# Kernel tuning notes

Hardware: AMD Instinct MI355X
Metric: run time of the kernel (lower is better)

The kernel has to match this reference:

```python
import jax, jax.numpy as jnp
import numpy as np

WINDOW = 8
HEADS = 8

def _rel_index(w):
    coords = np.stack(np.meshgrid(np.arange(w), np.arange(w), indexing='ij')).reshape(2, -1)
    rel = coords[:, :, None] - coords[:, None, :]          # [2, N, N]
    rel = rel.transpose(1, 2, 0) + (w - 1)                 # [N, N, 2]
    return jnp.asarray(rel[:, :, 0] * (2 * w - 1) + rel[:, :, 1])  # [N, N] int

def setup_inputs() -> dict:
    key = jax.random.key(0)
    ks = jax.random.split(key, 5)
    B, N, C = 4096, WINDOW * WINDOW, 256
    x = jax.random.normal(ks[0], (B, N, C), dtype=jnp.float32)
    w_qkv = jax.random.normal(ks[1], (3 * C, C), dtype=jnp.float32) * 0.02
    b_qkv = jnp.zeros((3 * C,), dtype=jnp.float32)
    bias_table = jax.random.normal(ks[2], ((2 * WINDOW - 1) ** 2, HEADS), dtype=jnp.float32) * 0.02
    w_proj = jax.random.normal(ks[3], (C, C), dtype=jnp.float32) * 0.02
    b_proj = jnp.zeros((C,), dtype=jnp.float32)
    return {"x": x, "w_qkv": w_qkv, "b_qkv": b_qkv, "bias_table": bias_table,
            "w_proj": w_proj, "b_proj": b_proj}

def reference(x, w_qkv, b_qkv, bias_table, w_proj, b_proj):
    B, N, C = x.shape
    H = HEADS
    d = C // H
    scale = d ** (-0.5)
    idx = _rel_index(WINDOW)                                # [N, N]
    qkv = x @ w_qkv.T + b_qkv                               # [B, N, 3C]
    qkv = qkv.reshape(B, N, 3, H, d).transpose(2, 0, 3, 1, 4)
    q, k, v = qkv[0], qkv[1], qkv[2]                        # [B, H, N, d]
    attn = jnp.einsum('bhnd,bhmd->bhnm', q * scale, k)      # [B, H, N, N]
    bias = bias_table[idx]                                  # [N, N, H]
    attn = attn + bias.transpose(2, 0, 1)[None]             # add per-head bias
    attn = jax.nn.softmax(attn, axis=-1)
    out = jnp.einsum('bhnm,bhmd->bhnd', attn, v)            # [B, H, N, d]
    out = out.transpose(0, 2, 1, 3).reshape(B, N, C)
    return out @ w_proj.T + b_proj
```

## Files before the change

### kernel.cpp

```cpp
#include <hip/hip_runtime.h>

typedef unsigned int u32;
typedef unsigned short u16;
typedef __bf16 bf16x8 __attribute__((ext_vector_type(8)));
typedef float f32x4 __attribute__((ext_vector_type(4)));
typedef u32 u32x4 __attribute__((ext_vector_type(4)));
typedef u32 u32x2 __attribute__((ext_vector_type(2)));

#define NTOK 64
#define CDIM 256
#define NH 8

#define WS_HDR 8
#define BIAS_O (WS_HDR)
#define WQKV_O (BIAS_O + 32768)
#define BQKV_O (WQKV_O + 196608)
#define WPRJ_O (BQKV_O + 768)
#define BPRJ_O (WPRJ_O + 65536)

#define XROW 520
#define LDS_BYTES 33280

__device__ __forceinline__ float bf2f(u16 u) {
  union { u32 i; float f; } z; z.i = ((u32)u) << 16; return z.f;
}
__device__ __forceinline__ u16 f2bf(float f) {
  __bf16 h = (__bf16)f; return __builtin_bit_cast(u16, h);
}
__device__ __forceinline__ u32 pk2(float a, float b) {
  return (u32)f2bf(a) | ((u32)f2bf(b) << 16);
}
__device__ __forceinline__ float fetchf(const void* p, int idx, int isbf) {
  return isbf ? bf2f(((const u16*)p)[idx]) : ((const float*)p)[idx];
}

__device__ __forceinline__ bf16x8 frag_from(u32 p00, u32 p01, u32 p10, u32 p11,
                                            int s0, int s1, bool hi) {
  u32 A0 = (u32)__shfl((int)p00, s0, 64);
  u32 A1 = (u32)__shfl((int)p01, s0, 64);
  u32 B0 = (u32)__shfl((int)p10, s0, 64);
  u32 B1 = (u32)__shfl((int)p11, s0, 64);
  u32 C0 = (u32)__shfl((int)p00, s1, 64);
  u32 C1 = (u32)__shfl((int)p01, s1, 64);
  u32 D0 = (u32)__shfl((int)p10, s1, 64);
  u32 D1 = (u32)__shfl((int)p11, s1, 64);
  u32x4 f;
  f[0] = hi ? B0 : A0;  f[1] = hi ? B1 : A1;
  f[2] = hi ? D0 : C0;  f[3] = hi ? D1 : C1;
  return __builtin_bit_cast(bf16x8, f);
}

__global__ void detect_dtype(const u16* __restrict__ x, int* __restrict__ flag) {
  __shared__ int cnt;
  if (threadIdx.x == 0) cnt = 0;
  __syncthreads();
  int sane = 0;
  for (int i = threadIdx.x; i < 2048; i += 256) {
    u16 u = x[2 * i];
    int e = (u >> 7) & 0xFF;
    sane += (e == 0 || (e >= 90 && e <= 160)) ? 1 : 0;
  }
  atomicAdd(&cnt, sane);
  __syncthreads();
  if (threadIdx.x == 0) *flag = (cnt >= 1638) ? 1 : 0;
}

__global__ void cvt_params(const void* __restrict__ wqkv, const void* __restrict__ bqkv,
                           const void* __restrict__ btab, const void* __restrict__ wprj,
                           const void* __restrict__ bprj, void* __restrict__ wsraw) {
  u16* ws = (u16*)wsraw;
  const int isbf = *(const int*)wsraw;
  int i = blockIdx.x * 256 + threadIdx.x;
  if (i < 32768) {
    int n = (i >> 6) & 63, m = i & 63, h = i >> 12;
    int r0 = (n >> 3) - (m >> 3) + 7, r1 = (n & 7) - (m & 7) + 7;
    ws[BIAS_O + i] = f2bf(fetchf(btab, (r0 * 15 + r1) * NH + h, isbf));
  } else if (i < 32768 + 196608) {
    int j = i - 32768;
    ws[WQKV_O + j] = f2bf(fetchf(wqkv, j, isbf));
  } else if (i < 32768 + 196608 + 768) {
    int j = i - (32768 + 196608);
    ws[BQKV_O + j] = f2bf(fetchf(bqkv, j, isbf));
  } else if (i < 32768 + 196608 + 768 + 65536) {
    int j = i - (32768 + 196608 + 768);
    ws[WPRJ_O + j] = f2bf(fetchf(wprj, j, isbf));
  } else if (i < 32768 + 196608 + 768 + 65536 + 256) {
    int j = i - (32768 + 196608 + 768 + 65536);
    ws[BPRJ_O + j] = f2bf(fetchf(bprj, j, isbf));
  }
}

#define TILE_T(PK, CHT, CHB, SCL) {                                                   \
    bf16x8 wf[8];                                                                     \
    const u16* wrow = ws + WQKV_O + ((CHB) + c) * CDIM;                               \
    _Pragma("unroll")                                                                 \
    for (int ks = 0; ks < 8; ++ks) wf[ks] = *(const bf16x8*)(wrow + ks * 32 + g * 8); \
    f32x4 binit;                                                                      \
    { u32x2 bp = *(const u32x2*)(ws + BQKV_O + (CHB) + 4 * g);                        \
      binit[0] = bf2f((u16)(bp[0] & 0xffff)); binit[1] = bf2f((u16)(bp[0] >> 16));    \
      binit[2] = bf2f((u16)(bp[1] & 0xffff)); binit[3] = bf2f((u16)(bp[1] >> 16)); }  \
    _Pragma("unroll")                                                                 \
    for (int nt = 0; nt < 4; ++nt) {                                                  \
      f32x4 acc = binit;                                                              \
      _Pragma("unroll")                                                               \
      for (int ks = 0; ks < 8; ++ks) {                                                \
        bf16x8 xf = *(const bf16x8*)(lds + (16 * nt + c) * XROW + ks * 64 + g * 16);  \
        acc = __builtin_amdgcn_mfma_f32_16x16x32_bf16(wf[ks], xf, acc, 0, 0, 0);      \
      }                                                                               \
      PK[CHT][nt][0] = pk2(acc[0] * (SCL), acc[1] * (SCL));                           \
      PK[CHT][nt][1] = pk2(acc[2] * (SCL), acc[3] * (SCL));                           \
    } }

#define TILE_N(PK, CHT, CHB) {                                                        \
    bf16x8 wf[8];                                                                     \
    const u16* wrow = ws + WQKV_O + ((CHB) + c) * CDIM;                               \
    _Pragma("unroll")                                                                 \
    for (int ks = 0; ks < 8; ++ks) wf[ks] = *(const bf16x8*)(wrow + ks * 32 + g * 8); \
    const float badd = bf2f(ws[BQKV_O + (CHB) + c]);                                  \
    _Pragma("unroll")                                                                 \
    for (int nt = 0; nt < 4; ++nt) {                                                  \
      f32x4 acc = {badd, badd, badd, badd};                                           \
      _Pragma("unroll")                                                               \
      for (int ks = 0; ks < 8; ++ks) {                                                \
        bf16x8 xf = *(const bf16x8*)(lds + (16 * nt + c) * XROW + ks * 64 + g * 16);  \
        acc = __builtin_amdgcn_mfma_f32_16x16x32_bf16(xf, wf[ks], acc, 0, 0, 0);      \
      }                                                                               \
      PK[CHT][nt][0] = pk2(acc[0], acc[1]);                                           \
      PK[CHT][nt][1] = pk2(acc[2], acc[3]);                                           \
    } }

__global__ __launch_bounds__(512, 3)
void win_attn_fused(const void* __restrict__ xraw, const void* __restrict__ wsraw,
                    float* __restrict__ out)
{
  __shared__ __align__(16) unsigned char lds[LDS_BYTES];
  const u16* ws  = (const u16*)wsraw;
  const int isbf = *(const int*)wsraw;
  const int b    = blockIdx.x;
  const int tid  = threadIdx.x;
  const int w    = tid >> 6;
  const int lane = tid & 63;
  const int c    = lane & 15;
  const int g    = lane >> 4;
  const float scale = 0.1767766952966369f;

  if (isbf) {
    const u32x4* gx = (const u32x4*)((const u16*)xraw + (size_t)b * (NTOK * CDIM));
#pragma unroll
    for (int i = 0; i < 4; ++i) {
      int q = tid + i * 512;
      int row = q >> 5, c8 = q & 31;
      *(u32x4*)(lds + row * XROW + c8 * 16) = gx[q];
    }
  } else {
    const f32x4* gx = (const f32x4*)((const float*)xraw + (size_t)b * (NTOK * CDIM));
#pragma unroll
    for (int i = 0; i < 8; ++i) {
      int q = tid + i * 512;
      int row = q >> 6, c4 = q & 63;
      f32x4 v = gx[q];
      u32x2 pkv;
      pkv[0] = pk2(v[0], v[1]);
      pkv[1] = pk2(v[2], v[3]);
      *(u32x2*)(lds + row * XROW + c4 * 8) = pkv;
    }
  }
  __syncthreads();

  const int s0 = c + 32 * (g & 1), s1 = s0 + 16;
  const bool hi = ((g >> 1) & 1) != 0;
  const int h = w;

  u32 qpk[2][4][2], kpk[2][4][2];
  bf16x8 bvf[2][2];
  TILE_T(qpk, 0, 32 * w,            scale);
  TILE_T(qpk, 1, 32 * w + 16,       scale);
  TILE_T(kpk, 0, 256 + 32 * w,      1.0f);
  TILE_T(kpk, 1, 256 + 32 * w + 16, 1.0f);
  {
    u32 vpk[2][4][2];
    TILE_N(vpk, 0, 512 + 32 * w);
    TILE_N(vpk, 1, 512 + 32 * w + 16);
#pragma unroll
    for (int dt = 0; dt < 2; ++dt)
#pragma unroll
      for (int k2 = 0; k2 < 2; ++k2)
        bvf[dt][k2] = frag_from(vpk[dt][2 * k2][0], vpk[dt][2 * k2][1],
                                vpk[dt][2 * k2 + 1][0], vpk[dt][2 * k2 + 1][1], s0, s1, hi);
  }
  __syncthreads();

  bf16x8 bkf[4];
#pragma unroll
  for (int mt = 0; mt < 4; ++mt)
    bkf[mt] = frag_from(kpk[0][mt][0], kpk[0][mt][1], kpk[1][mt][0], kpk[1][mt][1], s0, s1, hi);

#pragma unroll
  for (int nt = 0; nt < 4; ++nt) {
    bf16x8 aqf = frag_from(qpk[0][nt][0], qpk[0][nt][1], qpk[1][nt][0], qpk[1][nt][1], s0, s1, hi);
    f32x4 st[4];
#pragma unroll
    for (int mt = 0; mt < 4; ++mt) {
      u32x2 bp = *(const u32x2*)(ws + BIAS_O + (h << 12) + ((16 * nt + c) << 6) + 16 * mt + 4 * g);
      st[mt][0] = bf2f((u16)(bp[0] & 0xffff)); st[mt][1] = bf2f((u16)(bp[0] >> 16));
      st[mt][2] = bf2f((u16)(bp[1] & 0xffff)); st[mt][3] = bf2f((u16)(bp[1] >> 16));
    }
#pragma unroll
    for (int mt = 0; mt < 4; ++mt)
      st[mt] = __builtin_amdgcn_mfma_f32_16x16x32_bf16(bkf[mt], aqf, st[mt], 0, 0, 0);
    float mx = st[0][0];
#pragma unroll
    for (int mt = 0; mt < 4; ++mt)
#pragma unroll
      for (int r = 0; r < 4; ++r) mx = fmaxf(mx, st[mt][r]);
    mx = fmaxf(mx, __shfl_xor(mx, 16));
    mx = fmaxf(mx, __shfl_xor(mx, 32));
    float sum = 0.f;
#pragma unroll
    for (int mt = 0; mt < 4; ++mt)
#pragma unroll
      for (int r = 0; r < 4; ++r) { float e = __expf(st[mt][r] - mx); st[mt][r] = e; sum += e; }
    sum += __shfl_xor(sum, 16);
    sum += __shfl_xor(sum, 32);
    float inv = 1.0f / sum;
    u32 pp[4][2];
#pragma unroll
    for (int mt = 0; mt < 4; ++mt) {
      pp[mt][0] = pk2(st[mt][0] * inv, st[mt][1] * inv);
      pp[mt][1] = pk2(st[mt][2] * inv, st[mt][3] * inv);
    }
    f32x4 o2[2] = {{0,0,0,0},{0,0,0,0}};
#pragma unroll
    for (int k2 = 0; k2 < 2; ++k2) {
      bf16x8 paf = frag_from(pp[2 * k2][0], pp[2 * k2][1],
                             pp[2 * k2 + 1][0], pp[2 * k2 + 1][1], s0, s1, hi);
      o2[0] = __builtin_amdgcn_mfma_f32_16x16x32_bf16(paf, bvf[0][k2], o2[0], 0, 0, 0);
      o2[1] = __builtin_amdgcn_mfma_f32_16x16x32_bf16(paf, bvf[1][k2], o2[1], 0, 0, 0);
    }
#pragma unroll
    for (int dt = 0; dt < 2; ++dt)
#pragma unroll
      for (int r = 0; r < 4; ++r) {
        int n = 16 * nt + 4 * g + r, col = 32 * w + 16 * dt + c;
        *(u16*)(lds + n * XROW + col * 2) = f2bf(o2[dt][r]);
      }
  }
  __syncthreads();

  float* gout = out + (size_t)b * (NTOK * CDIM);
#pragma unroll
  for (int ct = 0; ct < 2; ++ct) {
    const int colw = 32 * w + 16 * ct + c;
    const float badd = bf2f(ws[BPRJ_O + colw]);
    f32x4 acc[4];
#pragma unroll
    for (int rt = 0; rt < 4; ++rt)
#pragma unroll
      for (int r = 0; r < 4; ++r) acc[rt][r] = badd;
    const u16* wrow = ws + WPRJ_O + colw * CDIM;
#pragma unroll
    for (int ks = 0; ks < 8; ++ks) {
      bf16x8 wf = *(const bf16x8*)(wrow + ks * 32 + g * 8);
#pragma unroll
      for (int rt = 0; rt < 4; ++rt) {
        bf16x8 ay = *(const bf16x8*)(lds + (16 * rt + c) * XROW + ks * 64 + g * 16);
        acc[rt] = __builtin_amdgcn_mfma_f32_16x16x32_bf16(ay, wf, acc[rt], 0, 0, 0);
      }
    }
#pragma unroll
    for (int rt = 0; rt < 4; ++rt)
#pragma unroll
      for (int r = 0; r < 4; ++r) {
        int n = 16 * rt + 4 * g + r;
        gout[n * CDIM + colw] = acc[rt][r];
      }
  }
}

extern "C" void kernel_launch(void* const* d_in, const int* in_sizes, int n_in,
                              void* d_out, int out_size, void* d_ws, size_t ws_size,
                              hipStream_t stream) {
  (void)in_sizes; (void)n_in; (void)out_size; (void)ws_size;
  detect_dtype<<<dim3(1), dim3(256), 0, stream>>>((const u16*)d_in[0], (int*)d_ws);
  cvt_params<<<dim3(1156), dim3(256), 0, stream>>>(d_in[1], d_in[2], d_in[3], d_in[4],
                                                   d_in[5], d_ws);
  win_attn_fused<<<dim3(4096), dim3(512), 0, stream>>>(d_in[0], d_ws, (float*)d_out);
}
```

Baseline: 495.3 us.

## Split fused window attention into QKV-attention and projection kernels via workspace

Replaces the single fused kernel with two kernels when the workspace is large enough. The first runs two 256-thread blocks per window, each handling four heads, and writes the bf16 attention output to a global workspace. The second reads it back and applies the output projection with 4 waves per block. The goal is smaller blocks with better occupancy and less register pressure. The cost is an extra global write and read of the intermediate (about 128 MB), the input x loaded twice, and each block redundantly loading x into LDS. The monolithic fallback now uses launch_bounds(512,2) instead of 3.

```diff
diff --git a/kernel.cpp b/kernel.cpp
--- a/kernel.cpp
+++ b/kernel.cpp
@@ -17,6 +17,8 @@
 #define BQKV_O (WQKV_O + 196608)
 #define WPRJ_O (BQKV_O + 768)
 #define BPRJ_O (WPRJ_O + 65536)
+#define Y_O    (BPRJ_O + 256)
+#define WS_NEED_BYTES ((size_t)(Y_O + 67108864) * 2)
 
 #define XROW 520
 #define LDS_BYTES 33280
@@ -129,9 +131,200 @@
       PK[CHT][nt][1] = pk2(acc[2], acc[3]);                                           \
     } }
 
-__global__ __launch_bounds__(512, 3)
-void win_attn_fused(const void* __restrict__ xraw, const void* __restrict__ wsraw,
-                    float* __restrict__ out)
+#define HEAD_BODY(H, SINK) {                                                          \
+    u32 qpk[2][4][2], kpk[2][4][2];                                                   \
+    bf16x8 bvf[2][2];                                                                 \
+    TILE_T(qpk, 0, 32 * (H),            scale);                                       \
+    TILE_T(qpk, 1, 32 * (H) + 16,       scale);                                       \
+    TILE_T(kpk, 0, 256 + 32 * (H),      1.0f);                                        \
+    TILE_T(kpk, 1, 256 + 32 * (H) + 16, 1.0f);                                        \
+    {                                                                                 \
+      u32 vpk[2][4][2];                                                               \
+      TILE_N(vpk, 0, 512 + 32 * (H));                                                 \
+      TILE_N(vpk, 1, 512 + 32 * (H) + 16);                                            \
+      _Pragma("unroll")                                                               \
+      for (int dt = 0; dt < 2; ++dt)                                                  \
+        _Pragma("unroll")                                                             \
+        for (int k2 = 0; k2 < 2; ++k2)                                                \
+          bvf[dt][k2] = frag_from(vpk[dt][2 * k2][0], vpk[dt][2 * k2][1],             \
+                                  vpk[dt][2 * k2 + 1][0], vpk[dt][2 * k2 + 1][1],     \
+                                  s0, s1, hi);                                        \
+    }                                                                                 \
+    bf16x8 bkf[4];                                                                    \
+    _Pragma("unroll")                                                                 \
+    for (int mt = 0; mt < 4; ++mt)                                                    \
+      bkf[mt] = frag_from(kpk[0][mt][0], kpk[0][mt][1], kpk[1][mt][0],                \
+                          kpk[1][mt][1], s0, s1, hi);                                 \
+    _Pragma("unroll")                                                                 \
+    for (int nt = 0; nt < 4; ++nt) {                                                  \
+      bf16x8 aqf = frag_from(qpk[0][nt][0], qpk[0][nt][1], qpk[1][nt][0],             \
+                             qpk[1][nt][1], s0, s1, hi);                              \
+      f32x4 st[4];                                                                    \
+      _Pragma("unroll")                                                               \
+      for (int mt = 0; mt < 4; ++mt) {                                                \
+        u32x2 bp = *(const u32x2*)(ws + BIAS_O + ((H) << 12) +                        \
+                                   ((16 * nt + c) << 6) + 16 * mt + 4 * g);           \
+        st[mt][0] = bf2f((u16)(bp[0] & 0xffff)); st[mt][1] = bf2f((u16)(bp[0] >> 16));\
+        st[mt][2] = bf2f((u16)(bp[1] & 0xffff)); st[mt][3] = bf2f((u16)(bp[1] >> 16));\
+      }                                                                               \
+      _Pragma("unroll")                                                               \
+      for (int mt = 0; mt < 4; ++mt)                                                  \
+        st[mt] = __builtin_amdgcn_mfma_f32_16x16x32_bf16(bkf[mt], aqf, st[mt], 0,0,0);\
+      float mx = st[0][0];                                                            \
+      _Pragma("unroll")                                                               \
+      for (int mt = 0; mt < 4; ++mt)                                                  \
+        _Pragma("unroll")                                                             \
+        for (int r = 0; r < 4; ++r) mx = fmaxf(mx, st[mt][r]);                        \
+      mx = fmaxf(mx, __shfl_xor(mx, 16));                                             \
+      mx = fmaxf(mx, __shfl_xor(mx, 32));                                             \
+      float sum = 0.f;                                                                \
+      _Pragma("unroll")                                                               \
+      for (int mt = 0; mt < 4; ++mt)                                                  \
+        _Pragma("unroll")                                                             \
+        for (int r = 0; r < 4; ++r) { float e = __expf(st[mt][r] - mx);               \
+                                      st[mt][r] = e; sum += e; }                      \
+      sum += __shfl_xor(sum, 16);                                                     \
+      sum += __shfl_xor(sum, 32);                                                     \
+      float inv = 1.0f / sum;                                                         \
+      u32 pp[4][2];                                                                   \
+      _Pragma("unroll")                                                               \
+      for (int mt = 0; mt < 4; ++mt) {                                                \
+        pp[mt][0] = pk2(st[mt][0] * inv, st[mt][1] * inv);                            \
+        pp[mt][1] = pk2(st[mt][2] * inv, st[mt][3] * inv);                            \
+      }                                                                               \
+      f32x4 o2[2] = {{0,0,0,0},{0,0,0,0}};                                            \
+      _Pragma("unroll")                                                               \
+      for (int k2 = 0; k2 < 2; ++k2) {                                                \
+        bf16x8 paf = frag_from(pp[2 * k2][0], pp[2 * k2][1],                          \
+                               pp[2 * k2 + 1][0], pp[2 * k2 + 1][1], s0, s1, hi);     \
+        o2[0] = __builtin_amdgcn_mfma_f32_16x16x32_bf16(paf, bvf[0][k2], o2[0],0,0,0);\
+        o2[1] = __builtin_amdgcn_mfma_f32_16x16x32_bf16(paf, bvf[1][k2], o2[1],0,0,0);\
+      }                                                                               \
+      SINK(H, nt, o2);                                                                \
+    } }
+
+
+#define SINK_YG(H, NT, O2) {                                                          \
+    _Pragma("unroll")                                                                 \
+    for (int dt = 0; dt < 2; ++dt)                                                    \
+      _Pragma("unroll")                                                               \
+      for (int r = 0; r < 4; ++r) {                                                   \
+        int n = 16 * (NT) + 4 * g + r, col = 32 * (H) + 16 * dt + c;                  \
+        yg[n * CDIM + col] = f2bf(O2[dt][r]);                                         \
+      } }
+
+__global__ __launch_bounds__(256, 3)
+void qkv_attn(const void* __restrict__ xraw, const void* __restrict__ wsraw,
+              u16* __restrict__ yws)
+{
+  __shared__ __align__(16) unsigned char lds[LDS_BYTES];
+  const u16* ws  = (const u16*)wsraw;
+  const int isbf = *(const int*)wsraw;
+  const int b    = blockIdx.x >> 1;
+  const int half = blockIdx.x & 1;
+  const int tid  = threadIdx.x;
+  const int w    = tid >> 6;
+  const int lane = tid & 63;
+  const int c    = lane & 15;
+  const int g    = lane >> 4;
+  const float scale = 0.1767766952966369f;
+
+  if (isbf) {
+    const u32x4* gx = (const u32x4*)((const u16*)xraw + (size_t)b * (NTOK * CDIM));
+#pragma unroll
+    for (int i = 0; i < 8; ++i) {
+      int q = tid + i * 256;
+      int row = q >> 5, c8 = q & 31;
+      *(u32x4*)(lds + row * XROW + c8 * 16) = gx[q];
+    }
+  } else {
+    const f32x4* gx = (const f32x4*)((const float*)xraw + (size_t)b * (NTOK * CDIM));
+#pragma unroll
+    for (int i = 0; i < 16; ++i) {
+      int q = tid + i * 256;
+      int row = q >> 6, c4 = q & 63;
+      f32x4 v = gx[q];
+      u32x2 pkv;
+      pkv[0] = pk2(v[0], v[1]);
+      pkv[1] = pk2(v[2], v[3]);
+      *(u32x2*)(lds + row * XROW + c4 * 8) = pkv;
+    }
+  }
+  __syncthreads();
+
+  const int s0 = c + 32 * (g & 1), s1 = s0 + 16;
+  const bool hi = ((g >> 1) & 1) != 0;
+  const int h = 4 * half + w;
+  u16* yg = yws + (size_t)b * (NTOK * CDIM);
+
+  HEAD_BODY(h, SINK_YG);
+}
+
+__global__ __launch_bounds__(256, 4)
+void proj_out(const u16* __restrict__ yws, const void* __restrict__ wsraw,
+              float* __restrict__ out)
+{
+  __shared__ __align__(16) unsigned char lds[LDS_BYTES];
+  const u16* ws  = (const u16*)wsraw;
+  const int b    = blockIdx.x;
+  const int tid  = threadIdx.x;
+  const int w    = tid >> 6;
+  const int lane = tid & 63;
+  const int c    = lane & 15;
+  const int g    = lane >> 4;
+
+  const u32x4* gy = (const u32x4*)(yws + (size_t)b * (NTOK * CDIM));
+#pragma unroll
+  for (int i = 0; i < 8; ++i) {
+    int q = tid + i * 256;
+    int row = q >> 5, c8 = q & 31;
+    *(u32x4*)(lds + row * XROW + c8 * 16) = gy[q];
+  }
+  __syncthreads();
+
+  float* gout = out + (size_t)b * (NTOK * CDIM);
+#pragma unroll
+  for (int ct = 0; ct < 4; ++ct) {
+    const int colw = 64 * w + 16 * ct + c;
+    const float badd = bf2f(ws[BPRJ_O + colw]);
+    f32x4 acc[4];
+#pragma unroll
+    for (int rt = 0; rt < 4; ++rt)
+#pragma unroll
+      for (int r = 0; r < 4; ++r) acc[rt][r] = badd;
+    const u16* wrow = ws + WPRJ_O + colw * CDIM;
+#pragma unroll
+    for (int ks = 0; ks < 8; ++ks) {
+      bf16x8 wf = *(const bf16x8*)(wrow + ks * 32 + g * 8);
+#pragma unroll
+      for (int rt = 0; rt < 4; ++rt) {
+        bf16x8 ay = *(const bf16x8*)(lds + (16 * rt + c) * XROW + ks * 64 + g * 16);
+        acc[rt] = __builtin_amdgcn_mfma_f32_16x16x32_bf16(ay, wf, acc[rt], 0, 0, 0);
+      }
+    }
+#pragma unroll
+    for (int rt = 0; rt < 4; ++rt)
+#pragma unroll
+      for (int r = 0; r < 4; ++r) {
+        int n = 16 * rt + 4 * g + r;
+        gout[n * CDIM + colw] = acc[rt][r];
+      }
+  }
+}
+
+
+#define SINK_LDSY(H, NT, O2) {                                                        \
+    _Pragma("unroll")                                                                 \
+    for (int dt = 0; dt < 2; ++dt)                                                    \
+      _Pragma("unroll")                                                               \
+      for (int r = 0; r < 4; ++r) {                                                   \
+        int n = 16 * (NT) + 4 * g + r, col = 32 * (H) + 16 * dt + c;                  \
+        *(u16*)(lds + n * XROW + col * 2) = f2bf(O2[dt][r]);                          \
+      } }
+
+__global__ __launch_bounds__(512, 2)
+void win_attn_mono(const void* __restrict__ xraw, const void* __restrict__ wsraw,
+                   float* __restrict__ out)
 {
   __shared__ __align__(16) unsigned char lds[LDS_BYTES];
   const u16* ws  = (const u16*)wsraw;
@@ -169,81 +362,76 @@
 
   const int s0 = c + 32 * (g & 1), s1 = s0 + 16;
   const bool hi = ((g >> 1) & 1) != 0;
-  const int h = w;
-
-  u32 qpk[2][4][2], kpk[2][4][2];
-  bf16x8 bvf[2][2];
-  TILE_T(qpk, 0, 32 * w,            scale);
-  TILE_T(qpk, 1, 32 * w + 16,       scale);
-  TILE_T(kpk, 0, 256 + 32 * w,      1.0f);
-  TILE_T(kpk, 1, 256 + 32 * w + 16, 1.0f);
+
   {
-    u32 vpk[2][4][2];
-    TILE_N(vpk, 0, 512 + 32 * w);
-    TILE_N(vpk, 1, 512 + 32 * w + 16);
-#pragma unroll
-    for (int dt = 0; dt < 2; ++dt)
-#pragma unroll
-      for (int k2 = 0; k2 < 2; ++k2)
-        bvf[dt][k2] = frag_from(vpk[dt][2 * k2][0], vpk[dt][2 * k2][1],
-                                vpk[dt][2 * k2 + 1][0], vpk[dt][2 * k2 + 1][1], s0, s1, hi);
-  }
-  __syncthreads();
-
-  bf16x8 bkf[4];
-#pragma unroll
-  for (int mt = 0; mt < 4; ++mt)
-    bkf[mt] = frag_from(kpk[0][mt][0], kpk[0][mt][1], kpk[1][mt][0], kpk[1][mt][1], s0, s1, hi);
-
-#pragma unroll
-  for (int nt = 0; nt < 4; ++nt) {
-    bf16x8 aqf = frag_from(qpk[0][nt][0], qpk[0][nt][1], qpk[1][nt][0], qpk[1][nt][1], s0, s1, hi);
-    f32x4 st[4];
-#pragma unroll
-    for (int mt = 0; mt < 4; ++mt) {
-      u32x2 bp = *(const u32x2*)(ws + BIAS_O + (h << 12) + ((16 * nt + c) << 6) + 16 * mt + 4 * g);
-      st[mt][0] = bf2f((u16)(bp[0] & 0xffff)); st[mt][1] = bf2f((u16)(bp[0] >> 16));
-      st[mt][2] = bf2f((u16)(bp[1] & 0xffff)); st[mt][3] = bf2f((u16)(bp[1] >> 16));
-    }
+    u32 qpk[2][4][2], kpk[2][4][2];
+    bf16x8 bvf[2][2];
+    TILE_T(qpk, 0, 32 * w,            scale);
+    TILE_T(qpk, 1, 32 * w + 16,       scale);
+    TILE_T(kpk, 0, 256 + 32 * w,      1.0f);
+    TILE_T(kpk, 1, 256 + 32 * w + 16, 1.0f);
+    {
+      u32 vpk[2][4][2];
+      TILE_N(vpk, 0, 512 + 32 * w);
+      TILE_N(vpk, 1, 512 + 32 * w + 16);
+#pragma unroll
+      for (int dt = 0; dt < 2; ++dt)
+#pragma unroll
+        for (int k2 = 0; k2 < 2; ++k2)
+          bvf[dt][k2] = frag_from(vpk[dt][2 * k2][0], vpk[dt][2 * k2][1],
+                                  vpk[dt][2 * k2 + 1][0], vpk[dt][2 * k2 + 1][1], s0, s1, hi);
+    }
+    __syncthreads();
+
+    bf16x8 bkf[4];
 #pragma unroll
     for (int mt = 0; mt < 4; ++mt)
-      st[mt] = __builtin_amdgcn_mfma_f32_16x16x32_bf16(bkf[mt], aqf, st[mt], 0, 0, 0);
-    float mx = st[0][0];
-#pragma unroll
-    for (int mt = 0; mt < 4; ++mt)
-#pragma unroll
-      for (int r = 0; r < 4; ++r) mx = fmaxf(mx, st[mt][r]);
-    mx = fmaxf(mx, __shfl_xor(mx, 16));
-    mx = fmaxf(mx, __shfl_xor(mx, 32));
-    float sum = 0.f;
-#pragma unroll
-    for (int mt = 0; mt < 4; ++mt)
-#pragma unroll
-      for (int r = 0; r < 4; ++r) { float e = __expf(st[mt][r] - mx); st[mt][r] = e; sum += e; }
-    sum += __shfl_xor(sum, 16);
-    sum += __shfl_xor(sum, 32);
-    float inv = 1.0f / sum;
-    u32 pp[4][2];
-#pragma unroll
-    for (int mt = 0; mt < 4; ++mt) {
-      pp[mt][0] = pk2(st[mt][0] * inv, st[mt][1] * inv);
-      pp[mt][1] = pk2(st[mt][2] * inv, st[mt][3] * inv);
-    }
-    f32x4 o2[2] = {{0,0,0,0},{0,0,0,0}};
-#pragma unroll
-    for (int k2 = 0; k2 < 2; ++k2) {
-      bf16x8 paf = frag_from(pp[2 * k2][0], pp[2 * k2][1],
-                             pp[2 * k2 + 1][0], pp[2 * k2 + 1][1], s0, s1, hi);
-      o2[0] = __builtin_amdgcn_mfma_f32_16x16x32_bf16(paf, bvf[0][k2], o2[0], 0, 0, 0);
-      o2[1] = __builtin_amdgcn_mfma_f32_16x16x32_bf16(paf, bvf[1][k2], o2[1], 0, 0, 0);
-    }
-#pragma unroll
-    for (int dt = 0; dt < 2; ++dt)
-#pragma unroll
-      for (int r = 0; r < 4; ++r) {
-        int n = 16 * nt + 4 * g + r, col = 32 * w + 16 * dt + c;
-        *(u16*)(lds + n * XROW + col * 2) = f2bf(o2[dt][r]);
-      }
+      bkf[mt] = frag_from(kpk[0][mt][0], kpk[0][mt][1], kpk[1][mt][0], kpk[1][mt][1], s0, s1, hi);
+
+#pragma unroll
+    for (int nt = 0; nt < 4; ++nt) {
+      bf16x8 aqf = frag_from(qpk[0][nt][0], qpk[0][nt][1], qpk[1][nt][0], qpk[1][nt][1], s0, s1, hi);
+      f32x4 st[4];
+#pragma unroll
+      for (int mt = 0; mt < 4; ++mt) {
+        u32x2 bp = *(const u32x2*)(ws + BIAS_O + (w << 12) + ((16 * nt + c) << 6) + 16 * mt + 4 * g);
+        st[mt][0] = bf2f((u16)(bp[0] & 0xffff)); st[mt][1] = bf2f((u16)(bp[0] >> 16));
+        st[mt][2] = bf2f((u16)(bp[1] & 0xffff)); st[mt][3] = bf2f((u16)(bp[1] >> 16));
+      }
+#pragma unroll
+      for (int mt = 0; mt < 4; ++mt)
+        st[mt] = __builtin_amdgcn_mfma_f32_16x16x32_bf16(bkf[mt], aqf, st[mt], 0, 0, 0);
+      float mx = st[0][0];
+#pragma unroll
+      for (int mt = 0; mt < 4; ++mt)
+#pragma unroll
+        for (int r = 0; r < 4; ++r) mx = fmaxf(mx, st[mt][r]);
+      mx = fmaxf(mx, __shfl_xor(mx, 16));
+      mx = fmaxf(mx, __shfl_xor(mx, 32));
+      float sum = 0.f;
+#pragma unroll
+      for (int mt = 0; mt < 4; ++mt)
+#pragma unroll
+        for (int r = 0; r < 4; ++r) { float e = __expf(st[mt][r] - mx); st[mt][r] = e; sum += e; }
+      sum += __shfl_xor(sum, 16);
+      sum += __shfl_xor(sum, 32);
+      float inv = 1.0f / sum;
+      u32 pp[4][2];
+#pragma unroll
+      for (int mt = 0; mt < 4; ++mt) {
+        pp[mt][0] = pk2(st[mt][0] * inv, st[mt][1] * inv);
+        pp[mt][1] = pk2(st[mt][2] * inv, st[mt][3] * inv);
+      }
+      f32x4 o2[2] = {{0,0,0,0},{0,0,0,0}};
+#pragma unroll
+      for (int k2 = 0; k2 < 2; ++k2) {
+        bf16x8 paf = frag_from(pp[2 * k2][0], pp[2 * k2][1],
+                               pp[2 * k2 + 1][0], pp[2 * k2 + 1][1], s0, s1, hi);
+        o2[0] = __builtin_amdgcn_mfma_f32_16x16x32_bf16(paf, bvf[0][k2], o2[0], 0, 0, 0);
+        o2[1] = __builtin_amdgcn_mfma_f32_16x16x32_bf16(paf, bvf[1][k2], o2[1], 0, 0, 0);
+      }
+      SINK_LDSY(w, nt, o2);
+    }
   }
   __syncthreads();
 
@@ -280,9 +468,15 @@
 extern "C" void kernel_launch(void* const* d_in, const int* in_sizes, int n_in,
                               void* d_out, int out_size, void* d_ws, size_t ws_size,
                               hipStream_t stream) {
-  (void)in_sizes; (void)n_in; (void)out_size; (void)ws_size;
+  (void)in_sizes; (void)n_in; (void)out_size;
   detect_dtype<<<dim3(1), dim3(256), 0, stream>>>((const u16*)d_in[0], (int*)d_ws);
   cvt_params<<<dim3(1156), dim3(256), 0, stream>>>(d_in[1], d_in[2], d_in[3], d_in[4],
                                                    d_in[5], d_ws);
-  win_attn_fused<<<dim3(4096), dim3(512), 0, stream>>>(d_in[0], d_ws, (float*)d_out);
-}
+  if (ws_size >= WS_NEED_BYTES) {
+    u16* yws = (u16*)d_ws + Y_O;
+    qkv_attn<<<dim3(8192), dim3(256), 0, stream>>>(d_in[0], d_ws, yws);
+    proj_out<<<dim3(4096), dim3(256), 0, stream>>>(yws, d_ws, (float*)d_out);
+  } else {
+    win_attn_mono<<<dim3(4096), dim3(512), 0, stream>>>(d_in[0], d_ws, (float*)d_out);
+  }
+}
```

Result: slower. 818.7 us (+65.3%).
